# Kernel optimization log

Hardware: AMD Instinct MI355X
Metric: run time of the kernel (lower is better)

Reference implementation:

```python
import jax, jax.numpy as jnp
import numpy as np

N = 100000      # nodes
E = 1600000     # edges
F_IN = 128
H = 128
L = 3           # GraphConv layers
C = 47          # classes
EPS = 1e-5      # BatchNorm eps


def setup_inputs() -> dict:
    key = jax.random.key(0)
    ks = jax.random.split(key, 12)
    feat = jax.random.normal(ks[0], (N, F_IN), dtype=jnp.float32)
    src = jax.random.randint(ks[1], (E,), 0, N, dtype=jnp.int32)
    dst = jax.random.randint(ks[2], (E,), 0, N, dtype=jnp.int32)
    s = 0.02
    W_in = jax.random.normal(ks[3], (F_IN, H), dtype=jnp.float32) * s
    b_in = jnp.zeros((H,), dtype=jnp.float32)
    Wc = jax.random.normal(ks[4], (L, H, H), dtype=jnp.float32) * s
    bc = jnp.zeros((L, H), dtype=jnp.float32)
    # BatchNorm (eval mode) params for layers+1 norms
    gamma = jnp.ones((L + 1, H), dtype=jnp.float32)
    beta = jnp.zeros((L + 1, H), dtype=jnp.float32)
    rmean = jax.random.normal(ks[5], (L + 1, H), dtype=jnp.float32) * 0.1
    rvar = jax.random.uniform(ks[6], (L + 1, H), dtype=jnp.float32, minval=0.5, maxval=1.5)
    W_out = jax.random.normal(ks[7], (H, C), dtype=jnp.float32) * s
    b_out = jnp.zeros((C,), dtype=jnp.float32)
    return {"feat": feat, "src": src, "dst": dst, "W_in": W_in, "b_in": b_in,
            "Wc": Wc, "bc": bc, "gamma": gamma, "beta": beta,
            "rmean": rmean, "rvar": rvar, "W_out": W_out, "b_out": b_out}


def _bn(x, g, b, m, v):
    # BatchNorm1d in eval mode (running stats)
    return (x - m) * jax.lax.rsqrt(v + EPS) * g + b


def _degree_norms(src, dst):
    ones = jnp.ones((E,), dtype=jnp.float32)
    deg_out = jax.ops.segment_sum(ones, src, num_segments=N)
    deg_in = jax.ops.segment_sum(ones, dst, num_segments=N)
    norm_src = jax.lax.rsqrt(jnp.maximum(deg_out, 1.0))
    norm_dst = jax.lax.rsqrt(jnp.maximum(deg_in, 1.0))
    return norm_src, norm_dst


def _graph_conv(h, src, dst, norm_src, norm_dst, W, b):
    # DGL GraphConv, norm='both': D_dst^{-1/2} A D_src^{-1/2} H W + b
    h = h * norm_src[:, None]
    agg = jax.ops.segment_sum(h[src], dst, num_segments=N)  # [N, H]
    agg = agg * norm_dst[:, None]
    return agg @ W + b


def reference(feat, src, dst, W_in, b_in, Wc, bc, gamma, beta, rmean, rvar, W_out, b_out):
    norm_src, norm_dst = _degree_norms(src, dst)
    h = feat @ W_in + b_in
    h = jax.nn.relu(_bn(h, gamma[0], beta[0], rmean[0], rvar[0]))
    # dropout is identity in eval mode
    for i in range(L):
        h = _graph_conv(h, src, dst, norm_src, norm_dst, Wc[i], bc[i])
        h = jax.nn.relu(_bn(h, gamma[i + 1], beta[i + 1], rmean[i + 1], rvar[i + 1]))
    return h @ W_out + b_out
```

## Files before the change

kernel.cpp:

```cpp
#include <hip/hip_runtime.h>
#include <cstddef>
#include <cstdint>

#define NN 100000
#define NE 1600000
#define HD 128
#define C_OUT 47
#define EPS_BN 1e-5f
#define SLAB 64
#define NCOPY 8

typedef _Float16 f16;
typedef __attribute__((ext_vector_type(2))) _Float16 f16x2;
typedef __attribute__((ext_vector_type(8))) _Float16 f16x8;
typedef __attribute__((ext_vector_type(4))) float f32x4;

__device__ inline ushort f16bits(f16 h) { return __builtin_bit_cast(ushort, h); }

__global__ __launch_bounds__(256) void k_build(
    const int* __restrict__ src, const int* __restrict__ dst,
    int* __restrict__ deg_out_c, int* __restrict__ cursor,
    int* __restrict__ slab) {
  int e = blockIdx.x * blockDim.x + threadIdx.x;
  if (e >= NE) return;
  int s = src[e], v = dst[e];
  atomicAdd(&deg_out_c[(blockIdx.x & (NCOPY - 1)) * NN + s], 1);
  int pos = atomicAdd(&cursor[v], 1);
  if (pos < SLAB) slab[(size_t)v * SLAB + pos] = s;
}

__global__ __launch_bounds__(256) void k_norms(
    const int* __restrict__ deg_out_c, const int* __restrict__ cursor,
    float* __restrict__ norm_src, float* __restrict__ norm_dst) {
  int v = blockIdx.x * blockDim.x + threadIdx.x;
  if (v >= NN) return;
  int d = 0;
  #pragma unroll
  for (int c = 0; c < NCOPY; ++c) d += deg_out_c[c * NN + v];
  norm_src[v] = rsqrtf((float)(d > 0 ? d : 1));
  int di = cursor[v];
  norm_dst[v] = rsqrtf((float)(di > 0 ? di : 1));
}

__global__ __launch_bounds__(256) void k_aggregate(
    const f16* __restrict__ h, const int* __restrict__ cursor,
    const int* __restrict__ slab, const float* __restrict__ norm_src,
    const float* __restrict__ norm_dst, f16* __restrict__ agg) {
  int wave = (int)((blockIdx.x * (unsigned)blockDim.x + threadIdx.x) >> 6);
  int lane = threadIdx.x & 63;
  if (wave >= NN) return;
  const f16x2* h2 = (const f16x2*)h;
  const int* cols = slab + (size_t)wave * SLAB;
  int d = cursor[wave];
  d = d < SLAB ? d : SLAB;
  float ax = 0.f, ay = 0.f;
  int j = 0;
  for (; j + 4 <= d; j += 4) {
    int u0 = cols[j + 0];
    int u1 = cols[j + 1];
    int u2 = cols[j + 2];
    int u3 = cols[j + 3];
    float w0 = norm_src[u0], w1 = norm_src[u1];
    float w2 = norm_src[u2], w3 = norm_src[u3];
    f16x2 x0 = h2[(size_t)u0 * 64 + lane];
    f16x2 x1 = h2[(size_t)u1 * 64 + lane];
    f16x2 x2 = h2[(size_t)u2 * 64 + lane];
    f16x2 x3 = h2[(size_t)u3 * 64 + lane];
    ax = fmaf(w0, (float)x0[0], ax); ay = fmaf(w0, (float)x0[1], ay);
    ax = fmaf(w1, (float)x1[0], ax); ay = fmaf(w1, (float)x1[1], ay);
    ax = fmaf(w2, (float)x2[0], ax); ay = fmaf(w2, (float)x2[1], ay);
    ax = fmaf(w3, (float)x3[0], ax); ay = fmaf(w3, (float)x3[1], ay);
  }
  for (; j < d; ++j) {
    int u = cols[j];
    float w = norm_src[u];
    f16x2 x = h2[(size_t)u * 64 + lane];
    ax = fmaf(w, (float)x[0], ax);
    ay = fmaf(w, (float)x[1], ay);
  }
  float nd = norm_dst[wave];
  f16x2 o;
  o[0] = (f16)(ax * nd);
  o[1] = (f16)(ay * nd);
  ((f16x2*)agg)[(size_t)wave * 64 + lane] = o;
}

template <bool A16>
__global__ __launch_bounds__(256, 2) void k_gemm128(
    const void* __restrict__ Av, const float* __restrict__ W,
    const float* __restrict__ bias, const float* __restrict__ gamma,
    const float* __restrict__ beta, const float* __restrict__ rmean,
    const float* __restrict__ rvar, f16* __restrict__ out) {
  __shared__ uint WtHi[128 * 64];
  __shared__ uint WtLo[128 * 64];
  int tid = threadIdx.x;
  for (int i = tid; i < 8192; i += 256) {
    int kp = i >> 7;
    int c = i & 127;
    int k = kp << 1;
    float w0 = W[(size_t)k * 128 + c];
    float w1 = W[(size_t)(k + 1) * 128 + c];
    f16 h0 = (f16)w0, h1 = (f16)w1;
    f16 l0 = (f16)(w0 - (float)h0), l1 = (f16)(w1 - (float)h1);
    int chunk = (k >> 3) ^ (c & 15);
    int ua = c * 64 + chunk * 4 + (kp & 3);
    WtHi[ua] = (uint)f16bits(h0) | ((uint)f16bits(h1) << 16);
    WtLo[ua] = (uint)f16bits(l0) | ((uint)f16bits(l1) << 16);
  }
  __syncthreads();

  int wv = tid >> 6, lane = tid & 63;
  int q = lane >> 4, m16 = lane & 15;
  int row_base = blockIdx.x * 128 + wv * 32;

  f32x4 acc[2][8];
  #pragma unroll
  for (int mt = 0; mt < 2; ++mt)
    #pragma unroll
    for (int nt = 0; nt < 8; ++nt)
      acc[mt][nt] = (f32x4){0.f, 0.f, 0.f, 0.f};

  #pragma unroll
  for (int kk = 0; kk < 4; ++kk) {
    f16x8 a[2];
    #pragma unroll
    for (int mt = 0; mt < 2; ++mt) {
      int r = row_base + mt * 16 + m16;
      r = r < NN ? r : NN - 1;
      if constexpr (A16) {
        a[mt] = *(const f16x8*)((const f16*)Av + (size_t)r * 128 + kk * 32 + q * 8);
      } else {
        const float4* ap = (const float4*)((const float*)Av + (size_t)r * 128 + kk * 32 + q * 8);
        float4 a0 = ap[0], a1 = ap[1];
        a[mt][0] = (f16)a0.x; a[mt][1] = (f16)a0.y;
        a[mt][2] = (f16)a0.z; a[mt][3] = (f16)a0.w;
        a[mt][4] = (f16)a1.x; a[mt][5] = (f16)a1.y;
        a[mt][6] = (f16)a1.z; a[mt][7] = (f16)a1.w;
      }
    }
    #pragma unroll
    for (int nt = 0; nt < 8; ++nt) {
      int n = nt * 16 + m16;
      int chunk = (kk * 4 + q) ^ m16;
      const f16x8 whi = *(const f16x8*)&WtHi[n * 64 + chunk * 4];
      const f16x8 wlo = *(const f16x8*)&WtLo[n * 64 + chunk * 4];
      #pragma unroll
      for (int mt = 0; mt < 2; ++mt) {
        acc[mt][nt] = __builtin_amdgcn_mfma_f32_16x16x32_f16(a[mt], whi, acc[mt][nt], 0, 0, 0);
        acc[mt][nt] = __builtin_amdgcn_mfma_f32_16x16x32_f16(a[mt], wlo, acc[mt][nt], 0, 0, 0);
      }
    }
  }

  float s[8], t[8];
  #pragma unroll
  for (int nt = 0; nt < 8; ++nt) {
    int col = nt * 16 + m16;
    float sc = gamma[col] * rsqrtf(rvar[col] + EPS_BN);
    s[nt] = sc;
    t[nt] = (bias[col] - rmean[col]) * sc + beta[col];
  }
  #pragma unroll
  for (int mt = 0; mt < 2; ++mt) {
    #pragma unroll
    for (int nt = 0; nt < 8; ++nt) {
      int col = nt * 16 + m16;
      #pragma unroll
      for (int e = 0; e < 4; ++e) {
        int r = row_base + mt * 16 + q * 4 + e;
        if (r < NN) {
          float y = fmaxf(acc[mt][nt][e] * s[nt] + t[nt], 0.f);
          out[(size_t)r * 128 + col] = (f16)y;
        }
      }
    }
  }
}

__global__ __launch_bounds__(256, 2) void k_gemm_out(
    const f16* __restrict__ A, const float* __restrict__ W,
    const float* __restrict__ bias, float* __restrict__ out) {
  __shared__ uint WtHi[48 * 64];
  __shared__ uint WtLo[48 * 64];
  int tid = threadIdx.x;
  for (int i = tid; i < 8192; i += 256) {
    int kp = i >> 7;
    int c = i & 127;
    if (c >= 48) continue;
    int k = kp << 1;
    float w0 = (c < C_OUT) ? W[(size_t)k * C_OUT + c] : 0.f;
    float w1 = (c < C_OUT) ? W[(size_t)(k + 1) * C_OUT + c] : 0.f;
    f16 h0 = (f16)w0, h1 = (f16)w1;
    f16 l0 = (f16)(w0 - (float)h0), l1 = (f16)(w1 - (float)h1);
    int chunk = (k >> 3) ^ (c & 15);
    int ua = c * 64 + chunk * 4 + (kp & 3);
    WtHi[ua] = (uint)f16bits(h0) | ((uint)f16bits(h1) << 16);
    WtLo[ua] = (uint)f16bits(l0) | ((uint)f16bits(l1) << 16);
  }
  __syncthreads();

  int wv = tid >> 6, lane = tid & 63;
  int q = lane >> 4, m16 = lane & 15;
  int row_base = blockIdx.x * 128 + wv * 32;

  f32x4 acc[2][3];
  #pragma unroll
  for (int mt = 0; mt < 2; ++mt)
    #pragma unroll
    for (int nt = 0; nt < 3; ++nt)
      acc[mt][nt] = (f32x4){0.f, 0.f, 0.f, 0.f};

  #pragma unroll
  for (int kk = 0; kk < 4; ++kk) {
    f16x8 a[2];
    #pragma unroll
    for (int mt = 0; mt < 2; ++mt) {
      int r = row_base + mt * 16 + m16;
      r = r < NN ? r : NN - 1;
      a[mt] = *(const f16x8*)(A + (size_t)r * 128 + kk * 32 + q * 8);
    }
    #pragma unroll
    for (int nt = 0; nt < 3; ++nt) {
      int n = nt * 16 + m16;
      int chunk = (kk * 4 + q) ^ m16;
      const f16x8 whi = *(const f16x8*)&WtHi[n * 64 + chunk * 4];
      const f16x8 wlo = *(const f16x8*)&WtLo[n * 64 + chunk * 4];
      #pragma unroll
      for (int mt = 0; mt < 2; ++mt) {
        acc[mt][nt] = __builtin_amdgcn_mfma_f32_16x16x32_f16(a[mt], whi, acc[mt][nt], 0, 0, 0);
        acc[mt][nt] = __builtin_amdgcn_mfma_f32_16x16x32_f16(a[mt], wlo, acc[mt][nt], 0, 0, 0);
      }
    }
  }

  #pragma unroll
  for (int nt = 0; nt < 3; ++nt) {
    int col = nt * 16 + m16;
    float b = (col < C_OUT) ? bias[col] : 0.f;
    #pragma unroll
    for (int mt = 0; mt < 2; ++mt) {
      #pragma unroll
      for (int e = 0; e < 4; ++e) {
        int r = row_base + mt * 16 + q * 4 + e;
        if (r < NN && col < C_OUT) {
          out[(size_t)r * C_OUT + col] = acc[mt][nt][e] + b;
        }
      }
    }
  }
}


extern "C" void kernel_launch(void* const* d_in, const int* in_sizes, int n_in,
                              void* d_out, int out_size, void* d_ws, size_t ws_size,
                              hipStream_t stream) {
  const float* feat = (const float*)d_in[0];
  const int* src = (const int*)d_in[1];
  const int* dst = (const int*)d_in[2];
  const float* W_in = (const float*)d_in[3];
  const float* b_in = (const float*)d_in[4];
  const float* Wc = (const float*)d_in[5];
  const float* bc = (const float*)d_in[6];
  const float* gamma = (const float*)d_in[7];
  const float* beta = (const float*)d_in[8];
  const float* rmean = (const float*)d_in[9];
  const float* rvar = (const float*)d_in[10];
  const float* W_out = (const float*)d_in[11];
  const float* b_out = (const float*)d_in[12];
  float* out = (float*)d_out;

  char* p = (char*)d_ws;
  f16* h = (f16*)p;             p += (size_t)NN * HD * sizeof(f16);
  f16* agg = (f16*)p;           p += (size_t)NN * HD * sizeof(f16);
  int* slab = (int*)p;          p += (size_t)NN * SLAB * sizeof(int);
  float* norm_src = (float*)p;  p += (size_t)NN * sizeof(float);
  float* norm_dst = (float*)p;  p += (size_t)NN * sizeof(float);
  int* deg_out_c = (int*)p;     p += (size_t)NCOPY * NN * sizeof(int);
  int* cursor = (int*)p;        p += (size_t)NN * sizeof(int);

  hipMemsetAsync(deg_out_c, 0, (size_t)(NCOPY + 1) * NN * sizeof(int), stream);

  k_build<<<(NE + 255) / 256, 256, 0, stream>>>(src, dst, deg_out_c, cursor, slab);
  k_norms<<<(NN + 255) / 256, 256, 0, stream>>>(deg_out_c, cursor, norm_src, norm_dst);

  int gblocks = (NN + 127) / 128;
  k_gemm128<false><<<gblocks, 256, 0, stream>>>(feat, W_in, b_in, gamma, beta,
                                                rmean, rvar, h);
  for (int l = 0; l < 3; ++l) {
    k_aggregate<<<(NN * 64 + 255) / 256, 256, 0, stream>>>(
        h, cursor, slab, norm_src, norm_dst, agg);
    k_gemm128<true><<<gblocks, 256, 0, stream>>>(
        agg, Wc + (size_t)l * HD * HD, bc + (size_t)l * HD,
        gamma + (size_t)(l + 1) * HD, beta + (size_t)(l + 1) * HD,
        rmean + (size_t)(l + 1) * HD, rvar + (size_t)(l + 1) * HD, h);
  }
  k_gemm_out<<<gblocks, 256, 0, stream>>>(h, W_out, b_out, out);
}
```

Baseline: 616.8 us.

## Store features in column-chunked layout and fold source norm into GEMM epilogue

```diff
diff --git a/kernel.cpp b/kernel.cpp
--- a/kernel.cpp
+++ b/kernel.cpp
@@ -9,9 +9,12 @@
 #define EPS_BN 1e-5f
 #define SLAB 64
 #define NCOPY 8
+#define CH 16
+#define NCH 8
+#define NPB 16
+#define BPC ((NN + NPB - 1) / NPB)
 
 typedef _Float16 f16;
-typedef __attribute__((ext_vector_type(2))) _Float16 f16x2;
 typedef __attribute__((ext_vector_type(8))) _Float16 f16x8;
 typedef __attribute__((ext_vector_type(4))) float f32x4;
 
@@ -44,45 +47,25 @@
 
 __global__ __launch_bounds__(256) void k_aggregate(
     const f16* __restrict__ h, const int* __restrict__ cursor,
-    const int* __restrict__ slab, const float* __restrict__ norm_src,
-    const float* __restrict__ norm_dst, f16* __restrict__ agg) {
-  int wave = (int)((blockIdx.x * (unsigned)blockDim.x + threadIdx.x) >> 6);
-  int lane = threadIdx.x & 63;
-  if (wave >= NN) return;
-  const f16x2* h2 = (const f16x2*)h;
-  const int* cols = slab + (size_t)wave * SLAB;
-  int d = cursor[wave];
+    const int* __restrict__ slab, const float* __restrict__ norm_dst,
+    f16* __restrict__ agg) {
+  int c = blockIdx.x / BPC;
+  int nb = blockIdx.x % BPC;
+  int g = threadIdx.x >> 4;
+  int l = threadIdx.x & 15;
+  int v = nb * NPB + g;
+  if (v >= NN) return;
+  const f16* hc = h + (size_t)c * NN * CH;
+  const int* cols = slab + (size_t)v * SLAB;
+  int d = cursor[v];
   d = d < SLAB ? d : SLAB;
-  float ax = 0.f, ay = 0.f;
-  int j = 0;
-  for (; j + 4 <= d; j += 4) {
-    int u0 = cols[j + 0];
-    int u1 = cols[j + 1];
-    int u2 = cols[j + 2];
-    int u3 = cols[j + 3];
-    float w0 = norm_src[u0], w1 = norm_src[u1];
-    float w2 = norm_src[u2], w3 = norm_src[u3];
-    f16x2 x0 = h2[(size_t)u0 * 64 + lane];
-    f16x2 x1 = h2[(size_t)u1 * 64 + lane];
-    f16x2 x2 = h2[(size_t)u2 * 64 + lane];
-    f16x2 x3 = h2[(size_t)u3 * 64 + lane];
-    ax = fmaf(w0, (float)x0[0], ax); ay = fmaf(w0, (float)x0[1], ay);
-    ax = fmaf(w1, (float)x1[0], ax); ay = fmaf(w1, (float)x1[1], ay);
-    ax = fmaf(w2, (float)x2[0], ax); ay = fmaf(w2, (float)x2[1], ay);
-    ax = fmaf(w3, (float)x3[0], ax); ay = fmaf(w3, (float)x3[1], ay);
-  }
-  for (; j < d; ++j) {
+  float acc = 0.f;
+  #pragma unroll 4
+  for (int j = 0; j < d; ++j) {
     int u = cols[j];
-    float w = norm_src[u];
-    f16x2 x = h2[(size_t)u * 64 + lane];
-    ax = fmaf(w, (float)x[0], ax);
-    ay = fmaf(w, (float)x[1], ay);
-  }
-  float nd = norm_dst[wave];
-  f16x2 o;
-  o[0] = (f16)(ax * nd);
-  o[1] = (f16)(ay * nd);
-  ((f16x2*)agg)[(size_t)wave * 64 + lane] = o;
+    acc += (float)hc[(size_t)u * CH + l];
+  }
+  agg[((size_t)c * NN + v) * CH + l] = (f16)(acc * norm_dst[v]);
 }
 
 template <bool A16>
@@ -90,7 +73,8 @@
     const void* __restrict__ Av, const float* __restrict__ W,
     const float* __restrict__ bias, const float* __restrict__ gamma,
     const float* __restrict__ beta, const float* __restrict__ rmean,
-    const float* __restrict__ rvar, f16* __restrict__ out) {
+    const float* __restrict__ rvar, const float* __restrict__ nsrc,
+    f16* __restrict__ out) {
   __shared__ uint WtHi[128 * 64];
   __shared__ uint WtLo[128 * 64];
   int tid = threadIdx.x;
@@ -128,7 +112,9 @@
       int r = row_base + mt * 16 + m16;
       r = r < NN ? r : NN - 1;
       if constexpr (A16) {
-        a[mt] = *(const f16x8*)((const f16*)Av + (size_t)r * 128 + kk * 32 + q * 8);
+        int ca = 2 * kk + (q >> 1);
+        int off = (q & 1) * 8;
+        a[mt] = *(const f16x8*)((const f16*)Av + ((size_t)ca * NN + r) * CH + off);
       } else {
         const float4* ap = (const float4*)((const float*)Av + (size_t)r * 128 + kk * 32 + q * 8);
         float4 a0 = ap[0], a1 = ap[1];
@@ -162,15 +148,20 @@
   }
   #pragma unroll
   for (int mt = 0; mt < 2; ++mt) {
+    float ns[4];
+    #pragma unroll
+    for (int e = 0; e < 4; ++e) {
+      int r = row_base + mt * 16 + q * 4 + e;
+      ns[e] = nsrc ? nsrc[r < NN ? r : NN - 1] : 1.f;
+    }
     #pragma unroll
     for (int nt = 0; nt < 8; ++nt) {
-      int col = nt * 16 + m16;
       #pragma unroll
       for (int e = 0; e < 4; ++e) {
         int r = row_base + mt * 16 + q * 4 + e;
         if (r < NN) {
-          float y = fmaxf(acc[mt][nt][e] * s[nt] + t[nt], 0.f);
-          out[(size_t)r * 128 + col] = (f16)y;
+          float y = fmaxf(acc[mt][nt][e] * s[nt] + t[nt], 0.f) * ns[e];
+          out[((size_t)nt * NN + r) * CH + m16] = (f16)y;
         }
       }
     }
@@ -217,7 +208,9 @@
     for (int mt = 0; mt < 2; ++mt) {
       int r = row_base + mt * 16 + m16;
       r = r < NN ? r : NN - 1;
-      a[mt] = *(const f16x8*)(A + (size_t)r * 128 + kk * 32 + q * 8);
+      int ca = 2 * kk + (q >> 1);
+      int off = (q & 1) * 8;
+      a[mt] = *(const f16x8*)(A + ((size_t)ca * NN + r) * CH + off);
     }
     #pragma unroll
     for (int nt = 0; nt < 3; ++nt) {
@@ -285,14 +278,14 @@
 
   int gblocks = (NN + 127) / 128;
   k_gemm128<false><<<gblocks, 256, 0, stream>>>(feat, W_in, b_in, gamma, beta,
-                                                rmean, rvar, h);
+                                                rmean, rvar, norm_src, h);
   for (int l = 0; l < 3; ++l) {
-    k_aggregate<<<(NN * 64 + 255) / 256, 256, 0, stream>>>(
-        h, cursor, slab, norm_src, norm_dst, agg);
+    k_aggregate<<<NCH * BPC, 256, 0, stream>>>(h, cursor, slab, norm_dst, agg);
+    const float* ns = (l < 2) ? norm_src : nullptr;
     k_gemm128<true><<<gblocks, 256, 0, stream>>>(
         agg, Wc + (size_t)l * HD * HD, bc + (size_t)l * HD,
         gamma + (size_t)(l + 1) * HD, beta + (size_t)(l + 1) * HD,
-        rmean + (size_t)(l + 1) * HD, rvar + (size_t)(l + 1) * HD, h);
+        rmean + (size_t)(l + 1) * HD, rvar + (size_t)(l + 1) * HD, ns, h);
   }
   k_gemm_out<<<gblocks, 256, 0, stream>>>(h, W_out, b_out, out);
 }
```

After: 862.4 us. 1.4x slower.
